# Optimization experiments

Hardware: AMD Instinct MI355X
Metric: run time of the kernel (lower is better)

The kernel has to match this reference:

```python
import jax, jax.numpy as jnp
import numpy as np

B, E, N, D, L = 16, 1024, 2048, 256, 3


def setup_inputs() -> dict:
    key = jax.random.key(0)
    ks = jax.random.split(key, 8)
    return {
        "evidences_mat": jax.random.normal(ks[0], (B, E, D), jnp.float32),
        "entities_mat": jax.random.normal(ks[1], (B, N, D), jnp.float32),
        "ev_to_ent": jax.random.bernoulli(ks[2], 0.05, (B, E, N)).astype(jnp.float32),
        "ent_to_ev": jax.random.bernoulli(ks[3], 0.05, (B, N, E)).astype(jnp.float32),
        "w_weight": jax.random.normal(ks[4], (L, D, D), jnp.float32) * 0.05,
        "w_bias": jax.random.normal(ks[5], (L, D), jnp.float32) * 0.05,
        "watt_weight": jax.random.normal(ks[6], (L, D, D), jnp.float32) * 0.05,
        "watt_bias": jax.random.normal(ks[7], (L, D), jnp.float32) * 0.05,
    }


def reference(evidences_mat, entities_mat, ev_to_ent, ent_to_ev,
              w_weight, w_bias, watt_weight, watt_bias):
    ev, ent = evidences_mat, entities_mat
    for i in range(L):
        # attention projections (torch Linear: x @ W.T + b)
        pe = jnp.einsum('bed,od->beo', ev, watt_weight[i]) + watt_bias[i]   # [B,E,D]
        pn = jnp.einsum('bnd,od->bno', ent, watt_weight[i]) + watt_bias[i]  # [B,N,D]
        # evidences -> entities messages
        ev_att = jnp.einsum('bed,bnd->ben', pe, pn) * ev_to_ent             # [B,E,N]
        ev_att = jax.nn.softmax(ev_att, axis=1)                              # over E (dim=1)
        msg_ent = jnp.einsum('ben,bed->bnd', ev_att, ev)                     # [B,N,D]
        msg_ent = jnp.einsum('bnd,od->bno', msg_ent, w_weight[i]) + w_bias[i]
        self_ent = jnp.einsum('bnd,od->bno', ent, w_weight[i]) + w_bias[i]
        ent = jax.nn.relu(msg_ent + self_ent)
        # entities -> evidences messages (uses UPDATED entities, as in source)
        ent_att = jnp.einsum('bnd,bed->bne', pn, pe) * ent_to_ev            # [B,N,E]
        ent_att = jax.nn.softmax(ent_att, axis=1)                            # over N (dim=1)
        msg_ev = jnp.einsum('bne,bnd->bed', ent_att, ent)                    # [B,E,D]
        msg_ev = jnp.einsum('bed,od->beo', msg_ev, w_weight[i]) + w_bias[i]
        self_ev = jnp.einsum('bed,od->beo', ev, w_weight[i]) + w_bias[i]
        ev = jax.nn.relu(msg_ev + self_ev)
        # dropout is a no-op (p=0.0 / eval)
    return ent, ev
```

## Files before the change

### kernel.cpp

```cpp
#include <hip/hip_runtime.h>

#define BB 16
#define EE 1024
#define NN 2048
#define DD 256
#define LL 3

typedef _Float16 half8 __attribute__((ext_vector_type(8)));
typedef _Float16 half4 __attribute__((ext_vector_type(4)));
typedef _Float16 half2_t __attribute__((ext_vector_type(2)));
typedef float f32x4 __attribute__((ext_vector_type(4)));

__device__ __forceinline__ void pmerge(float& m, float& s, float m2, float s2) {
    float nm = fmaxf(m, m2);
    s = s * __expf(m - nm) + s2 * __expf(m2 - nm);
    m = nm;
}

__device__ __forceinline__ unsigned pk2(_Float16 a, _Float16 b) {
    union { _Float16 h[2]; unsigned u; } x;
    x.h[0] = a; x.h[1] = b;
    return x.u;
}

__global__ void split_cast(const float* __restrict__ in, _Float16* __restrict__ hi,
                           _Float16* __restrict__ lo, size_t n) {
    size_t stride = (size_t)gridDim.x * blockDim.x * 4;
    for (size_t i = ((size_t)blockIdx.x * blockDim.x + threadIdx.x) * 4; i < n; i += stride) {
        float4 v = *(const float4*)&in[i];
        half4 hh, ll;
        _Float16 h;
        h = (_Float16)v.x; hh[0] = h; ll[0] = (_Float16)(v.x - (float)h);
        h = (_Float16)v.y; hh[1] = h; ll[1] = (_Float16)(v.y - (float)h);
        h = (_Float16)v.z; hh[2] = h; ll[2] = (_Float16)(v.z - (float)h);
        h = (_Float16)v.w; hh[3] = h; ll[3] = (_Float16)(v.w - (float)h);
        *(half4*)&hi[i] = hh;
        *(half4*)&lo[i] = ll;
    }
}

__global__ void cast_u8(const float* __restrict__ in, unsigned char* __restrict__ out, size_t n) {
    size_t stride = (size_t)gridDim.x * blockDim.x * 4;
    for (size_t i = ((size_t)blockIdx.x * blockDim.x + threadIdx.x) * 4; i < n; i += stride) {
        float4 v = *(const float4*)&in[i];
        unsigned int pack = (unsigned int)(unsigned char)v.x |
                            ((unsigned int)(unsigned char)v.y << 8) |
                            ((unsigned int)(unsigned char)v.z << 16) |
                            ((unsigned int)(unsigned char)v.w << 24);
        *(unsigned int*)&out[i] = pack;
    }
}

__global__ void transpose_split(const float* __restrict__ in, _Float16* __restrict__ oh,
                                _Float16* __restrict__ olo, int R, int C) {
    int b = blockIdx.z;
    int c0 = blockIdx.x * 64, r0 = blockIdx.y * 64;
    const float* ib = in + (size_t)b * R * C;
    size_t ob = (size_t)b * R * C;
    __shared__ float tile[64][65];
    int t = threadIdx.x;
    int cl = t & 63, rb = t >> 6;
#pragma unroll
    for (int j = 0; j < 16; j++) {
        int rl = rb + j * 4;
        tile[rl][cl] = ib[(size_t)(r0 + rl) * C + c0 + cl];
    }
    __syncthreads();
    int oc = t >> 2, q = t & 3;
    half8 h0, h1, l0, l1;
#pragma unroll
    for (int i = 0; i < 8; i++) {
        float v = tile[q * 16 + i][oc];
        _Float16 h = (_Float16)v;
        h0[i] = h; l0[i] = (_Float16)(v - (float)h);
    }
#pragma unroll
    for (int i = 0; i < 8; i++) {
        float v = tile[q * 16 + 8 + i][oc];
        _Float16 h = (_Float16)v;
        h1[i] = h; l1[i] = (_Float16)(v - (float)h);
    }
    size_t o = ob + (size_t)(c0 + oc) * R + r0 + q * 16;
    *(half8*)&oh[o] = h0; *(half8*)&oh[o + 8] = h1;
    *(half8*)&olo[o] = l0; *(half8*)&olo[o + 8] = l1;
}

__global__ void transpose_split_perm(const float* __restrict__ in, _Float16* __restrict__ oh,
                                     _Float16* __restrict__ olo, int R, int C) {
    int b = blockIdx.z;
    int c0 = blockIdx.x * 64, r0 = blockIdx.y * 64;
    const float* ib = in + (size_t)b * R * C;
    size_t ob = (size_t)b * R * C;
    __shared__ float tile[64][65];
    int t = threadIdx.x;
    int cl = t & 63, rb = t >> 6;
#pragma unroll
    for (int j = 0; j < 16; j++) {
        int rl = rb + j * 4;
        tile[rl][cl] = ib[(size_t)(r0 + rl) * C + c0 + cl];
    }
    __syncthreads();
    int oc = t >> 2, q = t & 3;
    int g = q >> 1, sub = q & 1;
#pragma unroll
    for (int j = 0; j < 8; j++) {
        int x = sub * 8 + j;
        float v1 = tile[g * 32 + x][oc];
        float v2 = tile[g * 32 + x + 16][oc];
        _Float16 a = (_Float16)v1, b2 = (_Float16)v2;
        _Float16 la = (_Float16)(v1 - (float)a), lb = (_Float16)(v2 - (float)b2);
        size_t o = ob + (size_t)(c0 + oc) * R + r0 + g * 32 + 2 * x;
        half2_t hp; hp[0] = a; hp[1] = b2;
        half2_t lp; lp[0] = la; lp[1] = lb;
        *(half2_t*)&oh[o] = hp;
        *(half2_t*)&olo[o] = lp;
    }
}

__global__ void transpose_u8(const float* __restrict__ in, unsigned char* __restrict__ out,
                             int R, int C) {
    int b = blockIdx.z;
    int c0 = blockIdx.x * 64, r0 = blockIdx.y * 64;
    const float* ib = in + (size_t)b * R * C;
    unsigned char* ob = out + (size_t)b * R * C;
    __shared__ float tile[64][65];
    int t = threadIdx.x;
    int cl = t & 63, rb = t >> 6;
#pragma unroll
    for (int j = 0; j < 16; j++) {
        int rl = rb + j * 4;
        tile[rl][cl] = ib[(size_t)(r0 + rl) * C + c0 + cl];
    }
    __syncthreads();
    int oc = t >> 2, q = t & 3;
    union { unsigned char b[16]; uint4 v; } u;
#pragma unroll
    for (int i = 0; i < 16; i++) u.b[i] = (unsigned char)tile[q * 16 + i][oc];
    size_t o = (size_t)(c0 + oc) * R + r0 + q * 16;
    *(uint4*)&ob[o] = u.v;
}

template <bool A_SPLIT, bool B_SPLIT, bool HAS_BIAS, bool RELU, bool HAS_ADD,
          bool WRITE_F32, bool WRITE_SPLIT, bool B_BATCHED>
__global__ __launch_bounds__(256) void gemm_nt(
    const _Float16* __restrict__ Ah, const _Float16* __restrict__ Al,
    const _Float16* __restrict__ Bh, const _Float16* __restrict__ Bl,
    const float* __restrict__ bias, float bscale,
    const float* __restrict__ addsrc,
    float* __restrict__ Cf, _Float16* __restrict__ Chi, _Float16* __restrict__ Clo,
    int M, int Nn, int K) {
    const int bz = blockIdx.z;
    const int m0 = blockIdx.x * 128, n0 = blockIdx.y * 128;
    const int t = threadIdx.x, lane = t & 63, wid = t >> 6;
    const int wm = wid >> 1, wn = wid & 1;
    const size_t offA = (size_t)bz * M * K;
    const size_t offB = B_BATCHED ? (size_t)bz * Nn * K : (size_t)0;
    const _Float16* Abh = Ah + offA;
    const _Float16* Abl = A_SPLIT ? (Al + offA) : nullptr;
    const _Float16* Bbh = Bh + offB;
    const _Float16* Bbl = B_SPLIT ? (Bl + offB) : nullptr;

    __shared__ _Float16 sAh[128 * 32];
    __shared__ _Float16 sBh[128 * 32];
    __shared__ _Float16 sAl[A_SPLIT ? 128 * 32 : 1];
    __shared__ _Float16 sBl[B_SPLIT ? 128 * 32 : 1];

    f32x4 acc[4][4] = {};
    const int nk = K >> 5;

    auto gA = [&](const _Float16* base, int kt, int q) {
        return *(const uint4*)(base + (size_t)(m0 + (q >> 2)) * K + (kt << 5) + ((q & 3) << 3));
    };
    auto gB = [&](const _Float16* base, int kt, int q) {
        return *(const uint4*)(base + (size_t)(n0 + (q >> 2)) * K + (kt << 5) + ((q & 3) << 3));
    };

    uint4 rah0 = gA(Abh, 0, t), rah1 = gA(Abh, 0, t + 256);
    uint4 rbh0 = gB(Bbh, 0, t), rbh1 = gB(Bbh, 0, t + 256);
    uint4 ral0 = {}, ral1 = {}, rbl0 = {}, rbl1 = {};
    if (A_SPLIT) { ral0 = gA(Abl, 0, t); ral1 = gA(Abl, 0, t + 256); }
    if (B_SPLIT) { rbl0 = gB(Bbl, 0, t); rbl1 = gB(Bbl, 0, t + 256); }

    for (int kt = 0; kt < nk; ++kt) {
        __syncthreads();
        ((uint4*)sAh)[t] = rah0; ((uint4*)sAh)[t + 256] = rah1;
        ((uint4*)sBh)[t] = rbh0; ((uint4*)sBh)[t + 256] = rbh1;
        if (A_SPLIT) { ((uint4*)sAl)[t] = ral0; ((uint4*)sAl)[t + 256] = ral1; }
        if (B_SPLIT) { ((uint4*)sBl)[t] = rbl0; ((uint4*)sBl)[t + 256] = rbl1; }
        __syncthreads();
        if (kt + 1 < nk) {
            rah0 = gA(Abh, kt + 1, t); rah1 = gA(Abh, kt + 1, t + 256);
            rbh0 = gB(Bbh, kt + 1, t); rbh1 = gB(Bbh, kt + 1, t + 256);
            if (A_SPLIT) { ral0 = gA(Abl, kt + 1, t); ral1 = gA(Abl, kt + 1, t + 256); }
            if (B_SPLIT) { rbl0 = gB(Bbl, kt + 1, t); rbl1 = gB(Bbl, kt + 1, t + 256); }
        }
        half8 afh[4], bfh[4], afl[4], bfl[4];
#pragma unroll
        for (int mi = 0; mi < 4; mi++) {
            int off = (wm * 64 + mi * 16 + (lane & 15)) * 32 + ((lane >> 4) << 3);
            afh[mi] = *(const half8*)&sAh[off];
            if (A_SPLIT) afl[mi] = *(const half8*)&sAl[off];
        }
#pragma unroll
        for (int nj = 0; nj < 4; nj++) {
            int off = (wn * 64 + nj * 16 + (lane & 15)) * 32 + ((lane >> 4) << 3);
            bfh[nj] = *(const half8*)&sBh[off];
            if (B_SPLIT) bfl[nj] = *(const half8*)&sBl[off];
        }
#pragma unroll
        for (int mi = 0; mi < 4; mi++)
#pragma unroll
            for (int nj = 0; nj < 4; nj++) {
                acc[mi][nj] = __builtin_amdgcn_mfma_f32_16x16x32_f16(afh[mi], bfh[nj], acc[mi][nj], 0, 0, 0);
                if (B_SPLIT)
                    acc[mi][nj] = __builtin_amdgcn_mfma_f32_16x16x32_f16(afh[mi], bfl[nj], acc[mi][nj], 0, 0, 0);
                if (A_SPLIT)
                    acc[mi][nj] = __builtin_amdgcn_mfma_f32_16x16x32_f16(afl[mi], bfh[nj], acc[mi][nj], 0, 0, 0);
            }
    }

    const int rbase = (lane >> 4) * 4, cc = lane & 15;
#pragma unroll
    for (int mi = 0; mi < 4; mi++) {
#pragma unroll
        for (int nj = 0; nj < 4; nj++) {
            int gn = n0 + wn * 64 + nj * 16 + cc;
            float bv = HAS_BIAS ? bias[gn] * bscale : 0.f;
#pragma unroll
            for (int r = 0; r < 4; r++) {
                int gm = m0 + wm * 64 + mi * 16 + rbase + r;
                float v = acc[mi][nj][r];
                if (HAS_BIAS) v += bv;
                size_t off = ((size_t)bz * M + gm) * Nn + gn;
                if (HAS_ADD) v += addsrc[off];
                if (RELU) v = fmaxf(v, 0.f);
                if (WRITE_F32) Cf[off] = v;
                if (WRITE_SPLIT) {
                    _Float16 h = (_Float16)v;
                    Chi[off] = h;
                    Clo[off] = (_Float16)(v - (float)h);
                }
            }
        }
    }
}

template <bool TRANSA>
__global__ __launch_bounds__(256) void fused_agg(
    const float* __restrict__ S_, const unsigned char* __restrict__ Mk,
    const float2* __restrict__ st, const _Float16* __restrict__ Bh,
    const _Float16* __restrict__ Bl, const float* __restrict__ addsrc,
    _Float16* __restrict__ Xhi, _Float16* __restrict__ Xlo,
    int M, int K) {
    const int bz = blockIdx.z;
    const int m0 = blockIdx.x * 128, n0 = blockIdx.y * 128;
    const int t = threadIdx.x, lane = t & 63, wid = t >> 6;
    const int wm = wid >> 1, wn = wid & 1;
    const float* Sb = S_ + (size_t)bz * EE * NN;
    const unsigned char* Mb = Mk + (size_t)bz * EE * NN;
    const float2* stb = st + (size_t)bz * M;
    const _Float16* Bbh = Bh + (size_t)bz * DD * K;
    const _Float16* Bbl = Bl + (size_t)bz * DD * K;

    __shared__ _Float16 sA[128 * 32];
    __shared__ _Float16 sBh[128 * 32];
    __shared__ _Float16 sBl[128 * 32];

    f32x4 acc[4][4] = {};
    const int nk = K >> 5;

    float stc[8], stem[8];
    if (TRANSA) {
        int ncol = (t & 15) * 4;
#pragma unroll
        for (int p = 0; p < 2; p++)
#pragma unroll
            for (int i = 0; i < 4; i++) {
                float2 v = stb[m0 + p * 64 + ncol + i];
                stc[p * 4 + i] = v.x; stem[p * 4 + i] = v.y;
            }
    } else {
#pragma unroll
        for (int p = 0; p < 4; p++) {
            float2 v = stb[m0 + (t >> 3) + p * 32];
            stc[p] = v.x; stem[p] = v.y;
        }
    }

    unsigned apack[8];
    uint4 rbh0, rbh1, rbl0, rbl1;

    auto prefA = [&](int kt) {
        if (TRANSA) {
            int r = t >> 4, ncol = (t & 15) * 4, e0 = kt * 32;
#pragma unroll
            for (int p = 0; p < 2; p++) {
                size_t rowoff = (size_t)(e0 + r) * NN + m0 + p * 64 + ncol;
                f32x4 s1 = *(const f32x4*)(Sb + rowoff);
                f32x4 s2 = *(const f32x4*)(Sb + rowoff + (size_t)16 * NN);
                unsigned a1 = *(const unsigned*)(Mb + rowoff);
                unsigned a2 = *(const unsigned*)(Mb + rowoff + (size_t)16 * NN);
#pragma unroll
                for (int i = 0; i < 4; i++) {
                    float c = stc[p * 4 + i], em = stem[p * 4 + i];
                    float x1 = ((a1 >> (8 * i)) & 255u) ? __expf(s1[i] - c) : em;
                    float x2 = ((a2 >> (8 * i)) & 255u) ? __expf(s2[i] - c) : em;
                    apack[p * 4 + i] = pk2((_Float16)x1, (_Float16)x2);
                }
            }
        } else {
            int kc = (t & 7) * 4, rb = t >> 3;
#pragma unroll
            for (int p = 0; p < 4; p++) {
                size_t rowoff = (size_t)(m0 + rb + p * 32) * NN + kt * 32 + kc;
                f32x4 s = *(const f32x4*)(Sb + rowoff);
                unsigned a = *(const unsigned*)(Mb + rowoff);
                float c = stc[p], em = stem[p];
                _Float16 h0 = (_Float16)(((a) & 255u) ? __expf(s[0] - c) : em);
                _Float16 h1 = (_Float16)(((a >> 8) & 255u) ? __expf(s[1] - c) : em);
                _Float16 h2 = (_Float16)(((a >> 16) & 255u) ? __expf(s[2] - c) : em);
                _Float16 h3 = (_Float16)(((a >> 24) & 255u) ? __expf(s[3] - c) : em);
                apack[2 * p] = pk2(h0, h1);
                apack[2 * p + 1] = pk2(h2, h3);
            }
        }
    };
    auto prefB = [&](int kt) {
        auto g = [&](const _Float16* base, int q) {
            return *(const uint4*)(base + (size_t)(n0 + (q >> 2)) * K + kt * 32 + (q & 3) * 8);
        };
        rbh0 = g(Bbh, t); rbh1 = g(Bbh, t + 256);
        rbl0 = g(Bbl, t); rbl1 = g(Bbl, t + 256);
    };
    auto storeAB = [&]() {
        if (TRANSA) {
            int r = t >> 4, ncol = (t & 15) * 4;
#pragma unroll
            for (int p = 0; p < 2; p++)
#pragma unroll
                for (int i = 0; i < 4; i++) {
                    int n = p * 64 + ncol + i;
                    int cp = (r >> 2) ^ ((n >> 2) & 3);
                    ((unsigned*)sA)[n * 16 + cp * 4 + (r & 3)] = apack[p * 4 + i];
                }
        } else {
            int kc = (t & 7) * 4, rb = t >> 3;
#pragma unroll
            for (int p = 0; p < 4; p++) {
                unsigned* dst = (unsigned*)&sA[(rb + p * 32) * 32 + kc];
                dst[0] = apack[2 * p]; dst[1] = apack[2 * p + 1];
            }
        }
        ((uint4*)sBh)[t] = rbh0; ((uint4*)sBh)[t + 256] = rbh1;
        ((uint4*)sBl)[t] = rbl0; ((uint4*)sBl)[t + 256] = rbl1;
    };

    prefA(0); prefB(0);

    for (int kt = 0; kt < nk; ++kt) {
        __syncthreads();
        storeAB();
        __syncthreads();
        if (kt + 1 < nk) { prefA(kt + 1); prefB(kt + 1); }
        half8 af[4], bfh[4], bfl[4];
        const int l4 = lane & 15, h = lane >> 4;
        const int cswz = TRANSA ? (h ^ ((l4 >> 2) & 3)) : h;
#pragma unroll
        for (int mi = 0; mi < 4; mi++)
            af[mi] = *(const half8*)&sA[(wm * 64 + mi * 16 + l4) * 32 + cswz * 8];
#pragma unroll
        for (int nj = 0; nj < 4; nj++) {
            int off = (wn * 64 + nj * 16 + l4) * 32 + h * 8;
            bfh[nj] = *(const half8*)&sBh[off];
            bfl[nj] = *(const half8*)&sBl[off];
        }
#pragma unroll
        for (int mi = 0; mi < 4; mi++)
#pragma unroll
            for (int nj = 0; nj < 4; nj++) {
                acc[mi][nj] = __builtin_amdgcn_mfma_f32_16x16x32_f16(af[mi], bfh[nj], acc[mi][nj], 0, 0, 0);
                acc[mi][nj] = __builtin_amdgcn_mfma_f32_16x16x32_f16(af[mi], bfl[nj], acc[mi][nj], 0, 0, 0);
            }
    }

    const int rbase = (lane >> 4) * 4, cc = lane & 15;
#pragma unroll
    for (int mi = 0; mi < 4; mi++) {
#pragma unroll
        for (int nj = 0; nj < 4; nj++) {
            int gn = n0 + wn * 64 + nj * 16 + cc;
#pragma unroll
            for (int r = 0; r < 4; r++) {
                int gm = m0 + wm * 64 + mi * 16 + rbase + r;
                size_t off = ((size_t)bz * M + gm) * DD + gn;
                float v = acc[mi][nj][r] + addsrc[off];
                _Float16 h = (_Float16)v;
                Xhi[off] = h;
                Xlo[off] = (_Float16)(v - (float)h);
            }
        }
    }
}

__global__ __launch_bounds__(256) void stats(const float* __restrict__ S_,
                                             const unsigned char* __restrict__ m1,
                                             const unsigned char* __restrict__ m2t,
                                             float2* __restrict__ d1p,
                                             float2* __restrict__ d2p) {
    int b = blockIdx.z, e0 = blockIdx.y * 64, n0 = blockIdx.x * 256;
    int t = threadIdx.x, lane = t & 63, w = t >> 6;
    size_t base = ((size_t)b * EE + e0) * NN + n0;

    f32x4 xs[16];
    unsigned int am[16], cm[16];
#pragma unroll
    for (int j = 0; j < 16; j++) {
        size_t off = base + (size_t)(w * 16 + j) * NN + lane * 4;
        float4 s = *(const float4*)(S_ + off);
        xs[j][0] = s.x; xs[j][1] = s.y; xs[j][2] = s.z; xs[j][3] = s.w;
        am[j] = *(const unsigned int*)(m1 + off);
        cm[j] = *(const unsigned int*)(m2t + off);
    }

    float cmx[4], csm[4];
#pragma unroll
    for (int i = 0; i < 4; i++) {
        float mx = ((am[0] >> (8 * i)) & 0xffu) ? xs[0][i] : 0.f;
#pragma unroll
        for (int j = 1; j < 16; j++) {
            float xe = ((am[j] >> (8 * i)) & 0xffu) ? xs[j][i] : 0.f;
            mx = fmaxf(mx, xe);
        }
        float sm = 0.f;
#pragma unroll
        for (int j = 0; j < 16; j++) {
            float xe = ((am[j] >> (8 * i)) & 0xffu) ? xs[j][i] : 0.f;
            sm += __expf(xe - mx);
        }
        cmx[i] = mx; csm[i] = sm;
    }
    __shared__ float rm[4][256], rs[4][256];
#pragma unroll
    for (int i = 0; i < 4; i++) { rm[w][lane * 4 + i] = cmx[i]; rs[w][lane * 4 + i] = csm[i]; }
    __syncthreads();
    {
        float M0 = rm[0][t], S0 = rs[0][t];
#pragma unroll
        for (int ww = 1; ww < 4; ww++) pmerge(M0, S0, rm[ww][t], rs[ww][t]);
        d1p[(size_t)blockIdx.y * (BB * NN) + (size_t)b * NN + n0 + t] = make_float2(M0, S0);
    }

#pragma unroll
    for (int j = 0; j < 16; j++) {
        float x0 = ((cm[j]) & 0xffu) ? xs[j][0] : 0.f;
        float x1 = ((cm[j] >> 8) & 0xffu) ? xs[j][1] : 0.f;
        float x2 = ((cm[j] >> 16) & 0xffu) ? xs[j][2] : 0.f;
        float x3 = ((cm[j] >> 24) & 0xffu) ? xs[j][3] : 0.f;
        float mx = fmaxf(fmaxf(x0, x1), fmaxf(x2, x3));
#pragma unroll
        for (int off = 1; off < 64; off <<= 1) mx = fmaxf(mx, __shfl_xor(mx, off, 64));
        float sm = __expf(x0 - mx) + __expf(x1 - mx) + __expf(x2 - mx) + __expf(x3 - mx);
#pragma unroll
        for (int off = 1; off < 64; off <<= 1) sm += __shfl_xor(sm, off, 64);
        if (lane == 0)
            d2p[(size_t)blockIdx.x * (BB * EE) + (size_t)b * EE + e0 + w * 16 + j] = make_float2(mx, sm);
    }
}

__global__ void reduce_dens(const float2* __restrict__ d1p, const float2* __restrict__ d2p,
                            float2* __restrict__ d1, float2* __restrict__ d2) {
    int i = blockIdx.x * 256 + threadIdx.x;
    if (i < BB * NN) {
        float2 v = d1p[i];
        float m = v.x, s = v.y;
#pragma unroll
        for (int k = 1; k < 16; k++) {
            float2 u = d1p[(size_t)k * (BB * NN) + i];
            pmerge(m, s, u.x, u.y);
        }
        float c = m + __logf(s);
        d1[i] = make_float2(c, __expf(-c));
    } else {
        int j = i - BB * NN;
        if (j < BB * EE) {
            float2 v = d2p[j];
            float m = v.x, s = v.y;
#pragma unroll
            for (int k = 1; k < 8; k++) {
                float2 u = d2p[(size_t)k * (BB * EE) + j];
                pmerge(m, s, u.x, u.y);
            }
            float c = m + __logf(s);
            d2[j] = make_float2(c, __expf(-c));
        }
    }
}

extern "C" void kernel_launch(void* const* d_in, const int* in_sizes, int n_in,
                              void* d_out, int out_size, void* d_ws, size_t ws_size,
                              hipStream_t stream) {
    const float* evid   = (const float*)d_in[0];
    const float* enti   = (const float*)d_in[1];
    const float* ev2ent = (const float*)d_in[2];
    const float* ent2ev = (const float*)d_in[3];
    const float* w_w    = (const float*)d_in[4];
    const float* w_b    = (const float*)d_in[5];
    const float* wa_w   = (const float*)d_in[6];
    const float* wa_b   = (const float*)d_in[7];
    float* out_ent = (float*)d_out;
    float* out_ev  = out_ent + (size_t)BB * NN * DD;

    char* p = (char*)d_ws;
    auto alloc = [&](size_t bytes) {
        char* r = p;
        p += (bytes + 255) & ~(size_t)255;
        return (void*)r;
    };
    const size_t nED = (size_t)BB * EE * DD, nND = (size_t)BB * NN * DD;
    const size_t nEN = (size_t)BB * EE * NN, nW = (size_t)LL * DD * DD;
    _Float16* Whi  = (_Float16*)alloc(nW * 2);
    _Float16* Wlo  = (_Float16*)alloc(nW * 2);
    _Float16* Wahi = (_Float16*)alloc(nW * 2);
    _Float16* Walo = (_Float16*)alloc(nW * 2);
    _Float16* evh  = (_Float16*)alloc(nED * 2);
    _Float16* evl  = (_Float16*)alloc(nED * 2);
    _Float16* enth = (_Float16*)alloc(nND * 2);
    _Float16* entl = (_Float16*)alloc(nND * 2);
    _Float16* evTh = (_Float16*)alloc(nED * 2);
    _Float16* evTl = (_Float16*)alloc(nED * 2);
    _Float16* entTh= (_Float16*)alloc(nND * 2);
    _Float16* entTl= (_Float16*)alloc(nND * 2);
    _Float16* peh  = (_Float16*)alloc(nED * 2);
    _Float16* pel  = (_Float16*)alloc(nED * 2);
    _Float16* pnh  = (_Float16*)alloc(nND * 2);
    _Float16* pnl  = (_Float16*)alloc(nND * 2);
    float*    S    = (float*)alloc(nEN * 4);
    unsigned char* m1  = (unsigned char*)alloc(nEN);
    unsigned char* m2t = (unsigned char*)alloc(nEN);
    float* evS  = (float*)alloc(nED * 4);
    float* entS = (float*)alloc(nND * 4);
    float2* d1p = (float2*)alloc((size_t)16 * BB * NN * 8);
    float2* d2p = (float2*)alloc((size_t)8 * BB * EE * 8);
    float2* d1  = (float2*)alloc((size_t)BB * NN * 8);
    float2* d2  = (float2*)alloc((size_t)BB * EE * 8);
    if ((size_t)(p - (char*)d_ws) > ws_size) return;
    _Float16* Xenth = pnh; _Float16* Xentl = pnl;
    _Float16* Xevh  = peh; _Float16* Xevl  = pel;

    split_cast<<<2048, 256, 0, stream>>>(wa_w, Wahi, Walo, nW);
    split_cast<<<2048, 256, 0, stream>>>(w_w, Whi, Wlo, nW);
    split_cast<<<2048, 256, 0, stream>>>(evid, evh, evl, nED);
    split_cast<<<2048, 256, 0, stream>>>(enti, enth, entl, nND);
    cast_u8<<<2048, 256, 0, stream>>>(ev2ent, m1, nEN);
    transpose_u8<<<dim3(EE / 64, NN / 64, BB), 256, 0, stream>>>(ent2ev, m2t, NN, EE);
    transpose_split_perm<<<dim3(DD / 64, EE / 64, BB), 256, 0, stream>>>(evid, evTh, evTl, EE, DD);
    hipMemcpyAsync(evS, evid, nED * 4, hipMemcpyDeviceToDevice, stream);
    hipMemcpyAsync(entS, enti, nND * 4, hipMemcpyDeviceToDevice, stream);

    for (int i = 0; i < LL; i++) {
        const _Float16* Wih  = Whi + (size_t)i * DD * DD;
        const _Float16* Wil  = Wlo + (size_t)i * DD * DD;
        const _Float16* Waih = Wahi + (size_t)i * DD * DD;
        const _Float16* Wail = Walo + (size_t)i * DD * DD;
        const float* bi  = w_b + i * DD;
        const float* bai = wa_b + i * DD;

        gemm_nt<true, true, true, false, false, false, true, false>
            <<<dim3(EE / 128, DD / 128, BB), 256, 0, stream>>>(
                evh, evl, Waih, Wail, bai, 1.f, nullptr, nullptr, peh, pel, EE, DD, DD);
        gemm_nt<true, true, true, false, false, false, true, false>
            <<<dim3(NN / 128, DD / 128, BB), 256, 0, stream>>>(
                enth, entl, Waih, Wail, bai, 1.f, nullptr, nullptr, pnh, pnl, NN, DD, DD);
        gemm_nt<true, true, false, false, false, true, false, true>
            <<<dim3(EE / 128, NN / 128, BB), 256, 0, stream>>>(
                peh, pel, pnh, pnl, nullptr, 0.f, nullptr, S, nullptr, nullptr, EE, NN, DD);
        stats<<<dim3(NN / 256, EE / 64, BB), 256, 0, stream>>>(S, m1, m2t, d1p, d2p);
        reduce_dens<<<(BB * NN + BB * EE + 255) / 256, 256, 0, stream>>>(d1p, d2p, d1, d2);
        fused_agg<true><<<dim3(NN / 128, 2, BB), 256, 0, stream>>>(
            S, m1, d1, evTh, evTl, entS, Xenth, Xentl, NN, EE);
        float* entDst = (i == LL - 1) ? out_ent : entS;
        gemm_nt<true, true, true, true, false, true, true, false>
            <<<dim3(NN / 128, DD / 128, BB), 256, 0, stream>>>(
                Xenth, Xentl, Wih, Wil, bi, 2.f, nullptr, entDst, enth, entl, NN, DD, DD);
        transpose_split<<<dim3(DD / 64, NN / 64, BB), 256, 0, stream>>>(entDst, entTh, entTl, NN, DD);
        fused_agg<false><<<dim3(EE / 128, 2, BB), 256, 0, stream>>>(
            S, m2t, d2, entTh, entTl, evS, Xevh, Xevl, EE, NN);
        float* evDst = (i == LL - 1) ? out_ev : evS;
        gemm_nt<true, true, true, true, false, true, true, false>
            <<<dim3(EE / 128, DD / 128, BB), 256, 0, stream>>>(
                Xevh, Xevl, Wih, Wil, bi, 2.f, nullptr, evDst, evh, evl, EE, DD, DD);
        if (i < LL - 1)
            transpose_split_perm<<<dim3(DD / 64, EE / 64, BB), 256, 0, stream>>>(evS, evTh, evTl, EE, DD);
    }
}
```

Baseline: 1.381 ms.

## Shrink fused_agg tile to 64x128 with 512 threads per block

Reworks the fused softmax-aggregation kernel to use 64-row M tiles with 8 waves of 2x2 MFMA fragments instead of 128-row tiles with 4 waves of 4x4 fragments. The grid doubles along M, and each thread handles far fewer prefetched values and accumulators, which raises parallelism and lowers register pressure. In exchange, the B tiles are reloaded twice as often, there is less MFMA work per shared-memory load, and the TRANSA path now uses scalar loads for S and the mask instead of vector loads.

```diff
diff --git a/kernel.cpp b/kernel.cpp
--- a/kernel.cpp
+++ b/kernel.cpp
@@ -246,113 +246,93 @@
 }
 
 template <bool TRANSA>
-__global__ __launch_bounds__(256) void fused_agg(
+__global__ __launch_bounds__(512) void fused_agg(
     const float* __restrict__ S_, const unsigned char* __restrict__ Mk,
     const float2* __restrict__ st, const _Float16* __restrict__ Bh,
     const _Float16* __restrict__ Bl, const float* __restrict__ addsrc,
     _Float16* __restrict__ Xhi, _Float16* __restrict__ Xlo,
     int M, int K) {
     const int bz = blockIdx.z;
-    const int m0 = blockIdx.x * 128, n0 = blockIdx.y * 128;
+    const int m0 = blockIdx.x * 64, n0 = blockIdx.y * 128;
     const int t = threadIdx.x, lane = t & 63, wid = t >> 6;
-    const int wm = wid >> 1, wn = wid & 1;
+    const int wm = wid >> 2, wn = wid & 3;
     const float* Sb = S_ + (size_t)bz * EE * NN;
     const unsigned char* Mb = Mk + (size_t)bz * EE * NN;
     const float2* stb = st + (size_t)bz * M;
     const _Float16* Bbh = Bh + (size_t)bz * DD * K;
     const _Float16* Bbl = Bl + (size_t)bz * DD * K;
 
-    __shared__ _Float16 sA[128 * 32];
+    __shared__ _Float16 sA[64 * 32];
     __shared__ _Float16 sBh[128 * 32];
     __shared__ _Float16 sBl[128 * 32];
 
-    f32x4 acc[4][4] = {};
+    f32x4 acc[2][2] = {};
     const int nk = K >> 5;
 
-    float stc[8], stem[8];
+    float stc[2], stem[2];
     if (TRANSA) {
-        int ncol = (t & 15) * 4;
-#pragma unroll
-        for (int p = 0; p < 2; p++)
-#pragma unroll
-            for (int i = 0; i < 4; i++) {
-                float2 v = stb[m0 + p * 64 + ncol + i];
-                stc[p * 4 + i] = v.x; stem[p * 4 + i] = v.y;
-            }
+        int c = t & 31;
+#pragma unroll
+        for (int i = 0; i < 2; i++) {
+            float2 v = stb[m0 + c + 32 * i];
+            stc[i] = v.x; stem[i] = v.y;
+        }
     } else {
-#pragma unroll
-        for (int p = 0; p < 4; p++) {
-            float2 v = stb[m0 + (t >> 3) + p * 32];
-            stc[p] = v.x; stem[p] = v.y;
-        }
-    }
-
-    unsigned apack[8];
-    uint4 rbh0, rbh1, rbl0, rbl1;
+        float2 v = stb[m0 + (t >> 3)];
+        stc[0] = v.x; stem[0] = v.y;
+    }
+
+    unsigned apack[2];
+    uint4 rbh, rbl;
 
     auto prefA = [&](int kt) {
         if (TRANSA) {
-            int r = t >> 4, ncol = (t & 15) * 4, e0 = kt * 32;
-#pragma unroll
-            for (int p = 0; p < 2; p++) {
-                size_t rowoff = (size_t)(e0 + r) * NN + m0 + p * 64 + ncol;
-                f32x4 s1 = *(const f32x4*)(Sb + rowoff);
-                f32x4 s2 = *(const f32x4*)(Sb + rowoff + (size_t)16 * NN);
-                unsigned a1 = *(const unsigned*)(Mb + rowoff);
-                unsigned a2 = *(const unsigned*)(Mb + rowoff + (size_t)16 * NN);
-#pragma unroll
-                for (int i = 0; i < 4; i++) {
-                    float c = stc[p * 4 + i], em = stem[p * 4 + i];
-                    float x1 = ((a1 >> (8 * i)) & 255u) ? __expf(s1[i] - c) : em;
-                    float x2 = ((a2 >> (8 * i)) & 255u) ? __expf(s2[i] - c) : em;
-                    apack[p * 4 + i] = pk2((_Float16)x1, (_Float16)x2);
-                }
+            int r = t >> 5, c = t & 31;
+            size_t ro1 = (size_t)(kt * 32 + r) * NN + m0;
+            size_t ro2 = ro1 + (size_t)16 * NN;
+#pragma unroll
+            for (int i = 0; i < 2; i++) {
+                int n = c + 32 * i;
+                float cst = stc[i], em = stem[i];
+                float x1 = Mb[ro1 + n] ? __expf(Sb[ro1 + n] - cst) : em;
+                float x2 = Mb[ro2 + n] ? __expf(Sb[ro2 + n] - cst) : em;
+                apack[i] = pk2((_Float16)x1, (_Float16)x2);
             }
         } else {
             int kc = (t & 7) * 4, rb = t >> 3;
-#pragma unroll
-            for (int p = 0; p < 4; p++) {
-                size_t rowoff = (size_t)(m0 + rb + p * 32) * NN + kt * 32 + kc;
-                f32x4 s = *(const f32x4*)(Sb + rowoff);
-                unsigned a = *(const unsigned*)(Mb + rowoff);
-                float c = stc[p], em = stem[p];
-                _Float16 h0 = (_Float16)(((a) & 255u) ? __expf(s[0] - c) : em);
-                _Float16 h1 = (_Float16)(((a >> 8) & 255u) ? __expf(s[1] - c) : em);
-                _Float16 h2 = (_Float16)(((a >> 16) & 255u) ? __expf(s[2] - c) : em);
-                _Float16 h3 = (_Float16)(((a >> 24) & 255u) ? __expf(s[3] - c) : em);
-                apack[2 * p] = pk2(h0, h1);
-                apack[2 * p + 1] = pk2(h2, h3);
-            }
+            size_t rowoff = (size_t)(m0 + rb) * NN + kt * 32 + kc;
+            f32x4 s = *(const f32x4*)(Sb + rowoff);
+            unsigned a = *(const unsigned*)(Mb + rowoff);
+            float c = stc[0], em = stem[0];
+            _Float16 h0 = (_Float16)(((a) & 255u) ? __expf(s[0] - c) : em);
+            _Float16 h1 = (_Float16)(((a >> 8) & 255u) ? __expf(s[1] - c) : em);
+            _Float16 h2 = (_Float16)(((a >> 16) & 255u) ? __expf(s[2] - c) : em);
+            _Float16 h3 = (_Float16)(((a >> 24) & 255u) ? __expf(s[3] - c) : em);
+            apack[0] = pk2(h0, h1);
+            apack[1] = pk2(h2, h3);
         }
     };
     auto prefB = [&](int kt) {
-        auto g = [&](const _Float16* base, int q) {
-            return *(const uint4*)(base + (size_t)(n0 + (q >> 2)) * K + kt * 32 + (q & 3) * 8);
+        auto g = [&](const _Float16* base) {
+            return *(const uint4*)(base + (size_t)(n0 + (t >> 2)) * K + kt * 32 + (t & 3) * 8);
         };
-        rbh0 = g(Bbh, t); rbh1 = g(Bbh, t + 256);
-        rbl0 = g(Bbl, t); rbl1 = g(Bbl, t + 256);
+        rbh = g(Bbh); rbl = g(Bbl);
     };
     auto storeAB = [&]() {
         if (TRANSA) {
-            int r = t >> 4, ncol = (t & 15) * 4;
-#pragma unroll
-            for (int p = 0; p < 2; p++)
-#pragma unroll
-                for (int i = 0; i < 4; i++) {
-                    int n = p * 64 + ncol + i;
-                    int cp = (r >> 2) ^ ((n >> 2) & 3);
-                    ((unsigned*)sA)[n * 16 + cp * 4 + (r & 3)] = apack[p * 4 + i];
-                }
+            int r = t >> 5, c = t & 31;
+#pragma unroll
+            for (int i = 0; i < 2; i++) {
+                int n = c + 32 * i;
+                int cp = (r >> 2) ^ ((n >> 2) & 3);
+                ((unsigned*)sA)[n * 16 + cp * 4 + (r & 3)] = apack[i];
+            }
         } else {
             int kc = (t & 7) * 4, rb = t >> 3;
-#pragma unroll
-            for (int p = 0; p < 4; p++) {
-                unsigned* dst = (unsigned*)&sA[(rb + p * 32) * 32 + kc];
-                dst[0] = apack[2 * p]; dst[1] = apack[2 * p + 1];
-            }
-        }
-        ((uint4*)sBh)[t] = rbh0; ((uint4*)sBh)[t + 256] = rbh1;
-        ((uint4*)sBl)[t] = rbl0; ((uint4*)sBl)[t + 256] = rbl1;
+            unsigned* dst = (unsigned*)&sA[rb * 32 + kc];
+            dst[0] = apack[0]; dst[1] = apack[1];
+        }
+        ((uint4*)sBh)[t] = rbh; ((uint4*)sBl)[t] = rbl;
     };
 
     prefA(0); prefB(0);
@@ -362,22 +342,22 @@
         storeAB();
         __syncthreads();
         if (kt + 1 < nk) { prefA(kt + 1); prefB(kt + 1); }
-        half8 af[4], bfh[4], bfl[4];
+        half8 af[2], bfh[2], bfl[2];
         const int l4 = lane & 15, h = lane >> 4;
         const int cswz = TRANSA ? (h ^ ((l4 >> 2) & 3)) : h;
 #pragma unroll
-        for (int mi = 0; mi < 4; mi++)
-            af[mi] = *(const half8*)&sA[(wm * 64 + mi * 16 + l4) * 32 + cswz * 8];
-#pragma unroll
-        for (int nj = 0; nj < 4; nj++) {
-            int off = (wn * 64 + nj * 16 + l4) * 32 + h * 8;
+        for (int mi = 0; mi < 2; mi++)
+            af[mi] = *(const half8*)&sA[(wm * 32 + mi * 16 + l4) * 32 + cswz * 8];
+#pragma unroll
+        for (int nj = 0; nj < 2; nj++) {
+            int off = (wn * 32 + nj * 16 + l4) * 32 + h * 8;
             bfh[nj] = *(const half8*)&sBh[off];
             bfl[nj] = *(const half8*)&sBl[off];
         }
 #pragma unroll
-        for (int mi = 0; mi < 4; mi++)
-#pragma unroll
-            for (int nj = 0; nj < 4; nj++) {
+        for (int mi = 0; mi < 2; mi++)
+#pragma unroll
+            for (int nj = 0; nj < 2; nj++) {
                 acc[mi][nj] = __builtin_amdgcn_mfma_f32_16x16x32_f16(af[mi], bfh[nj], acc[mi][nj], 0, 0, 0);
                 acc[mi][nj] = __builtin_amdgcn_mfma_f32_16x16x32_f16(af[mi], bfl[nj], acc[mi][nj], 0, 0, 0);
             }
@@ -385,13 +365,13 @@
 
     const int rbase = (lane >> 4) * 4, cc = lane & 15;
 #pragma unroll
-    for (int mi = 0; mi < 4; mi++) {
-#pragma unroll
-        for (int nj = 0; nj < 4; nj++) {
-            int gn = n0 + wn * 64 + nj * 16 + cc;
+    for (int mi = 0; mi < 2; mi++) {
+#pragma unroll
+        for (int nj = 0; nj < 2; nj++) {
+            int gn = n0 + wn * 32 + nj * 16 + cc;
 #pragma unroll
             for (int r = 0; r < 4; r++) {
-                int gm = m0 + wm * 64 + mi * 16 + rbase + r;
+                int gm = m0 + wm * 32 + mi * 16 + rbase + r;
                 size_t off = ((size_t)bz * M + gm) * DD + gn;
                 float v = acc[mi][nj][r] + addsrc[off];
                 _Float16 h = (_Float16)v;
@@ -576,14 +556,14 @@
                 peh, pel, pnh, pnl, nullptr, 0.f, nullptr, S, nullptr, nullptr, EE, NN, DD);
         stats<<<dim3(NN / 256, EE / 64, BB), 256, 0, stream>>>(S, m1, m2t, d1p, d2p);
         reduce_dens<<<(BB * NN + BB * EE + 255) / 256, 256, 0, stream>>>(d1p, d2p, d1, d2);
-        fused_agg<true><<<dim3(NN / 128, 2, BB), 256, 0, stream>>>(
+        fused_agg<true><<<dim3(NN / 64, 2, BB), 512, 0, stream>>>(
             S, m1, d1, evTh, evTl, entS, Xenth, Xentl, NN, EE);
         float* entDst = (i == LL - 1) ? out_ent : entS;
         gemm_nt<true, true, true, true, false, true, true, false>
             <<<dim3(NN / 128, DD / 128, BB), 256, 0, stream>>>(
                 Xenth, Xentl, Wih, Wil, bi, 2.f, nullptr, entDst, enth, entl, NN, DD, DD);
         transpose_split<<<dim3(DD / 64, NN / 64, BB), 256, 0, stream>>>(entDst, entTh, entTl, NN, DD);
-        fused_agg<false><<<dim3(EE / 128, 2, BB), 256, 0, stream>>>(
+        fused_agg<false><<<dim3(EE / 64, 2, BB), 512, 0, stream>>>(
             S, m2t, d2, entTh, entTl, evS, Xevh, Xevl, EE, NN);
         float* evDst = (i == LL - 1) ? out_ev : evS;
         gemm_nt<true, true, true, true, false, true, true, false>
```

After: 1.716 ms. +24.2%, slower.
